# Performance work log

Hardware: AMD Instinct MI355X
Metric: run time of the kernel (lower is better)

Reference implementation:

```python
import jax, jax.numpy as jnp
import numpy as np

B, N, K = 4, 4096, 16
DP, DM = 128, 256  # d_points, d_model


def setup_inputs() -> dict:
    key = jax.random.key(0)
    ks = jax.random.split(key, 10)
    w = lambda k, s: (jax.random.normal(k, s) * 0.02).astype(jnp.float32)
    return dict(
        features=jax.random.normal(ks[0], (B, N, DP), dtype=jnp.float32),
        xyz=jax.random.normal(ks[1], (B, N, 3), dtype=jnp.float32),
        fc1_w=w(ks[2], (DP, DM)), fc1_b=jnp.zeros((DM,), jnp.float32),
        fc2_w=w(ks[3], (DM, DP)), fc2_b=jnp.zeros((DP,), jnp.float32),
        fd1_w=w(ks[4], (3, DM)), fd1_b=jnp.zeros((DM,), jnp.float32),
        fd2_w=w(ks[5], (DM, DM)), fd2_b=jnp.zeros((DM,), jnp.float32),
        wq=w(ks[6], (DM, DM)), wk=w(ks[7], (DM, DM)), wv=w(ks[8], (DM, DM)),
    )


def reference(features, xyz, fc1_w, fc1_b, fc2_w, fc2_b,
              fd1_w, fd1_b, fd2_w, fd2_b, wq, wk, wv):
    # KNN of xyz against itself (includes self, distance-sorted ascending)
    sq = jnp.sum(xyz * xyz, axis=-1)                                 # [B,N]
    d2 = sq[:, :, None] + sq[:, None, :] - 2.0 * jnp.einsum('bnc,bmc->bnm', xyz, xyz)
    _, knn_idx = jax.lax.top_k(-d2, K)                               # [B,N,K]
    gather = jax.vmap(lambda pts, idx: pts[idx])                     # [B,N,C],[B,N,K]->[B,N,K,C]
    knn_xyz = gather(xyz, knn_idx)                                   # [B,N,K,3]

    x = features @ fc1_w + fc1_b                                     # [B,N,DM]
    q = x @ wq                                                       # [B,N,DM]
    kf = gather(x @ wk, knn_idx)                                     # [B,N,K,DM]
    vf = gather(x @ wv, knn_idx)                                     # [B,N,K,DM]

    delta = xyz[:, :, None, :] - knn_xyz                             # [B,N,K,3]
    pos = jax.nn.relu(delta @ fd1_w + fd1_b) @ fd2_w + fd2_b         # [B,N,K,DM]

    logits = jnp.einsum('bnd,bnkd->bnk', q, kf + pos) / np.sqrt(DM).astype(np.float32)
    attn = jax.nn.softmax(logits, axis=-1)                           # [B,N,K]
    res = jnp.einsum('bnk,bnkd->bnd', attn, vf + pos)                # [B,N,DM]

    out = res @ fc2_w + fc2_b + features                             # [B,N,DP]
    return jnp.transpose(out, (0, 2, 1))                             # [B,DP,N]
```

## Files before the change

kernel.cpp:

```cpp
#include <hip/hip_runtime.h>
#include <hip/hip_bf16.h>
#include <math.h>

#define B_   4
#define N_   4096
#define K_   16
#define DP_  128
#define DM_  256
#define NPTS (B_ * N_)
#define SEG_ 16
#define CAND_ (N_ / SEG_)
#define QPAD 136

typedef unsigned int u32;
typedef unsigned char u8;
typedef _Float16 f16;
typedef __attribute__((ext_vector_type(2))) __fp16 h2;
typedef __attribute__((ext_vector_type(8))) _Float16 f16x8;
typedef __attribute__((ext_vector_type(4))) float floatx4;

static __device__ __forceinline__ h2 pkrtz(float a, float b) {
    return __builtin_amdgcn_cvt_pkrtz(a, b);
}
static __device__ __forceinline__ u32 asu32(h2 h) { return __builtin_bit_cast(u32, h); }
static __device__ __forceinline__ h2 ash2(u32 u) { return __builtin_bit_cast(h2, u); }

#define CEXA(x, y) { u32 _lo = min(x, y); y = max(x, y); x = _lo; }
#define CEXD(x, y) { u32 _hi = max(x, y); y = min(x, y); x = _hi; }

static __device__ __forceinline__ void sort16_desc(u32 c[16]) {
    CEXD(c[0],c[1]);  CEXA(c[2],c[3]);  CEXD(c[4],c[5]);  CEXA(c[6],c[7]);
    CEXD(c[8],c[9]);  CEXA(c[10],c[11]); CEXD(c[12],c[13]); CEXA(c[14],c[15]);

    CEXD(c[0],c[2]);  CEXD(c[1],c[3]);  CEXA(c[4],c[6]);  CEXA(c[5],c[7]);
    CEXD(c[8],c[10]); CEXD(c[9],c[11]); CEXA(c[12],c[14]); CEXA(c[13],c[15]);
    CEXD(c[0],c[1]);  CEXD(c[2],c[3]);  CEXA(c[4],c[5]);  CEXA(c[6],c[7]);
    CEXD(c[8],c[9]);  CEXD(c[10],c[11]); CEXA(c[12],c[13]); CEXA(c[14],c[15]);

    CEXD(c[0],c[4]);  CEXD(c[1],c[5]);  CEXD(c[2],c[6]);  CEXD(c[3],c[7]);
    CEXA(c[8],c[12]); CEXA(c[9],c[13]); CEXA(c[10],c[14]); CEXA(c[11],c[15]);
    CEXD(c[0],c[2]);  CEXD(c[1],c[3]);  CEXD(c[4],c[6]);  CEXD(c[5],c[7]);
    CEXA(c[8],c[10]); CEXA(c[9],c[11]); CEXA(c[12],c[14]); CEXA(c[13],c[15]);
    CEXD(c[0],c[1]);  CEXD(c[2],c[3]);  CEXD(c[4],c[5]);  CEXD(c[6],c[7]);
    CEXA(c[8],c[9]);  CEXA(c[10],c[11]); CEXA(c[12],c[13]); CEXA(c[14],c[15]);

    CEXD(c[0],c[8]);  CEXD(c[1],c[9]);  CEXD(c[2],c[10]); CEXD(c[3],c[11]);
    CEXD(c[4],c[12]); CEXD(c[5],c[13]); CEXD(c[6],c[14]); CEXD(c[7],c[15]);
    CEXD(c[0],c[4]);  CEXD(c[1],c[5]);  CEXD(c[2],c[6]);  CEXD(c[3],c[7]);
    CEXD(c[8],c[12]); CEXD(c[9],c[13]); CEXD(c[10],c[14]); CEXD(c[11],c[15]);
    CEXD(c[0],c[2]);  CEXD(c[1],c[3]);  CEXD(c[4],c[6]);  CEXD(c[5],c[7]);
    CEXD(c[8],c[10]); CEXD(c[9],c[11]); CEXD(c[12],c[14]); CEXD(c[13],c[15]);
    CEXD(c[0],c[1]);  CEXD(c[2],c[3]);  CEXD(c[4],c[5]);  CEXD(c[6],c[7]);
    CEXD(c[8],c[9]);  CEXD(c[10],c[11]); CEXD(c[12],c[13]); CEXD(c[14],c[15]);
}

static __device__ __forceinline__ void remerge16_asc(u32 L[16]) {
    CEXA(L[0],L[8]);  CEXA(L[1],L[9]);  CEXA(L[2],L[10]); CEXA(L[3],L[11]);
    CEXA(L[4],L[12]); CEXA(L[5],L[13]); CEXA(L[6],L[14]); CEXA(L[7],L[15]);
    CEXA(L[0],L[4]);  CEXA(L[1],L[5]);  CEXA(L[2],L[6]);  CEXA(L[3],L[7]);
    CEXA(L[8],L[12]); CEXA(L[9],L[13]); CEXA(L[10],L[14]); CEXA(L[11],L[15]);
    CEXA(L[0],L[2]);  CEXA(L[1],L[3]);  CEXA(L[4],L[6]);  CEXA(L[5],L[7]);
    CEXA(L[8],L[10]); CEXA(L[9],L[11]); CEXA(L[12],L[14]); CEXA(L[13],L[15]);
    CEXA(L[0],L[1]);  CEXA(L[2],L[3]);  CEXA(L[4],L[5]);  CEXA(L[6],L[7]);
    CEXA(L[8],L[9]);  CEXA(L[10],L[11]); CEXA(L[12],L[13]); CEXA(L[14],L[15]);
}

static __device__ void knn_part_body(float4* sc, const float* __restrict__ xyz,
                                     u32* __restrict__ part, int id)
{
    const int xblk = id & 15;
    const int s = (id >> 4) & 15;
    const int b = id >> 8;
    const int n = xblk * 256 + threadIdx.x;
    const float* xb = xyz + (size_t)b * N_ * 3;
    const float nx0 = -xb[n * 3 + 0], nx1 = -xb[n * 3 + 1], nx2 = -xb[n * 3 + 2];
    const u32 kmask = 0xFFFFF000u;

    {
        const int m = s * CAND_ + threadIdx.x;
        const float a0 = xb[m * 3 + 0];
        const float a1 = xb[m * 3 + 1];
        const float a2 = xb[m * 3 + 2];
        sc[threadIdx.x] = make_float4(a0, a1, a2, 0.5f * (a0 * a0 + a1 * a1 + a2 * a2));
    }
    __syncthreads();

    u32 L[16];
#pragma unroll
    for (int i = 0; i < 16; ++i) L[i] = 0xFFFFFFFFu;

    const u32 ibase = (u32)(s * CAND_);
    for (int m0 = 0; m0 < CAND_; m0 += 16) {
        u32 c[16];
#pragma unroll
        for (int t = 0; t < 16; ++t) {
            const float4 cc = sc[m0 + t];
            const float e = fmaf(nx0, cc.x, fmaf(nx1, cc.y, fmaf(nx2, cc.z, cc.w)));
            const int ib = __float_as_int(e);
            const u32 tk = (u32)ib ^ (u32)((ib >> 31) | 0x80000000);
            c[t] = (tk & kmask) | (ibase + (u32)(m0 + t));
        }
        sort16_desc(c);
#pragma unroll
        for (int i = 0; i < 16; ++i) L[i] = min(L[i], c[i]);
        remerge16_asc(L);
    }

    const int p = b * N_ + n;
#pragma unroll
    for (int j = 0; j < 16; ++j)
        part[(size_t)(s * 16 + j) * NPTS + p] = L[j];
}

static __device__ void prep_body(float (*t)[33],
    const float* __restrict__ wq, const float* __restrict__ wk, const float* __restrict__ wv,
    const float* __restrict__ fd2, const float* __restrict__ fc1, const float* __restrict__ fc2,
    const float* __restrict__ feat,
    f16* __restrict__ catW, f16* __restrict__ fc2T, f16* __restrict__ bt2,
    f16* __restrict__ fd2c, f16* __restrict__ wqc, f16* __restrict__ fc1c,
    f16* __restrict__ featb, int bx, int by, int job)
{
    const int tid = threadIdx.x;

    if (job < 4) {
        const float* in; int R, C;
        switch (job) {
            case 0: in = wq;  R = DM_; C = DM_; break;
            case 1: in = wk;  R = DM_; C = DM_; break;
            case 2: in = wv;  R = DM_; C = DM_; break;
            default: in = fc2; R = DM_; C = DP_; break;
        }
        const int c0 = bx * 32, r0 = by * 32;
        if (c0 >= C || r0 >= R) return;
        const int lx = tid & 31, ly = tid >> 5;
#pragma unroll
        for (int i = 0; i < 32; i += 8)
            t[ly + i][lx] = in[(size_t)(r0 + ly + i) * C + c0 + lx];
        __syncthreads();
#pragma unroll
        for (int i = 0; i < 32; i += 8) {
            const int c = c0 + ly + i;
            const f16 v = (f16)t[lx][ly + i];
            int n;
            switch (job) {
                case 0: n = c; break;
                case 1: n = 256 + ((c >> 2) << 3) + (c & 3); break;
                case 2: n = 256 + ((c >> 2) << 3) + 4 + (c & 3); break;
                default: n = -1; break;
            }
            if (job < 3) {
                catW[(size_t)n * DM_ + r0 + lx] = v;
            } else {
                fc2T[(size_t)c * DM_ + r0 + lx] = v;
                bt2[(size_t)c * 512 + 256 + r0 + lx] = v;
            }
        }
    } else {
        const int bid = by * 8 + bx;
        const int tId = bid * 256 + tid;
        const float* in; f16* outp; int n4;
        if (job == 4)      { in = fd2;  outp = fd2c;  n4 = (DM_ * DM_) / 4; }
        else if (job == 5) { in = wq;   outp = wqc;   n4 = (DM_ * DM_) / 4; }
        else if (job == 6) { in = fc1;  outp = fc1c;  n4 = (DP_ * DM_) / 4; }
        else               { in = feat; outp = featb; n4 = (NPTS * DP_) / 4; }
        for (int i = tId; i < n4; i += 16384) {
            const float4 v = ((const float4*)in)[i];
            const u32 lo = asu32(pkrtz(v.x, v.y));
            const u32 hi = asu32(pkrtz(v.z, v.w));
            ((uint2*)outp)[i] = make_uint2(lo, hi);
        }
    }
}

__global__ __launch_bounds__(256) void fused_prep_knn_kernel(
    const float* __restrict__ wq, const float* __restrict__ wk, const float* __restrict__ wv,
    const float* __restrict__ fd2, const float* __restrict__ fc1, const float* __restrict__ fc2,
    const float* __restrict__ feat,
    f16* __restrict__ catW, f16* __restrict__ fc2T, f16* __restrict__ bt2,
    f16* __restrict__ fd2c, f16* __restrict__ wqc, f16* __restrict__ fc1c,
    f16* __restrict__ featb,
    const float* __restrict__ xyz, u32* __restrict__ part)
{
    __shared__ __align__(16) char smem[4352];
    const int id = blockIdx.x;
    if (id < 512) {
        prep_body((float(*)[33])smem, wq, wk, wv, fd2, fc1, fc2, feat,
                  catW, fc2T, bt2, fd2c, wqc, fc1c, featb,
                  id & 7, (id >> 3) & 7, id >> 6);
    } else {
        knn_part_body((float4*)smem, xyz, part, id - 512);
    }
}

static __device__ void gemm_tile(f16* As, f16* Bs,
    const f16* __restrict__ A, const f16* __restrict__ Bt,
    f16* __restrict__ Cb,
    int M, int N, int K, int ldc, int bx, int by)
{
    const int tid = threadIdx.x;
    const int m0 = by * 128, n0 = bx * 128;
    const int w = tid >> 6, l = tid & 63;
    const int wm = (w >> 1) * 64, wn = (w & 1) * 64;
    const int fm = l & 15, kq = l >> 4;

    floatx4 acc[4][4];
#pragma unroll
    for (int i = 0; i < 4; ++i)
#pragma unroll
        for (int j = 0; j < 4; ++j)
            acc[i][j] = (floatx4){0.0f, 0.0f, 0.0f, 0.0f};

    for (int k0 = 0; k0 < K; k0 += 32) {
        __syncthreads();
#pragma unroll
        for (int c = 0; c < 2; ++c) {
            const int li = tid + c * 256;
            const int row = li >> 2, part = li & 3;
            *(uint4*)&As[row * 32 + part * 8] =
                *(const uint4*)&A[(size_t)(m0 + row) * K + k0 + part * 8];
            *(uint4*)&Bs[row * 32 + part * 8] =
                *(const uint4*)&Bt[(size_t)(n0 + row) * K + k0 + part * 8];
        }
        __syncthreads();
        f16x8 af[4], bf[4];
#pragma unroll
        for (int i = 0; i < 4; ++i)
            af[i] = *(const f16x8*)&As[(wm + i * 16 + fm) * 32 + kq * 8];
#pragma unroll
        for (int j = 0; j < 4; ++j)
            bf[j] = *(const f16x8*)&Bs[(wn + j * 16 + fm) * 32 + kq * 8];
#pragma unroll
        for (int i = 0; i < 4; ++i)
#pragma unroll
            for (int j = 0; j < 4; ++j)
                acc[i][j] = __builtin_amdgcn_mfma_f32_16x16x32_f16(af[i], bf[j], acc[i][j], 0, 0, 0);
    }

#pragma unroll
    for (int i = 0; i < 4; ++i) {
#pragma unroll
        for (int j = 0; j < 4; ++j) {
            const int col = n0 + wn + j * 16 + fm;
            const int rowb = m0 + wm + i * 16 + kq * 4;
#pragma unroll
            for (int r = 0; r < 4; ++r)
                Cb[(size_t)(rowb + r) * ldc + col] = (f16)acc[i][j][r];
        }
    }
}

__global__ __launch_bounds__(256) void gemm_qkv_kernel(
    const f16* __restrict__ A,
    const f16* __restrict__ Bt,
    const float* __restrict__ bias,
    f16* __restrict__ Cb)
{
    __shared__ __align__(16) f16 As[128 * QPAD];
    __shared__ __align__(16) f16 Bs[128 * QPAD];
    const int tid = threadIdx.x;
    const int m0 = blockIdx.y * 128, n0 = blockIdx.x * 128;
    const int w = tid >> 6, l = tid & 63;
    const int wm = (w >> 1) * 64, wn = (w & 1) * 64;
    const int fm = l & 15, kq = l >> 4;

#pragma unroll
    for (int c = 0; c < 8; ++c) {
        const int li = tid + c * 256;
        const int row = li >> 4, part = li & 15;
        *(uint4*)&As[row * QPAD + part * 8] =
            *(const uint4*)&A[(size_t)(m0 + row) * 128 + part * 8];
        *(uint4*)&Bs[row * QPAD + part * 8] =
            *(const uint4*)&Bt[(size_t)(n0 + row) * 128 + part * 8];
    }
    __syncthreads();

    floatx4 acc[4][4];
#pragma unroll
    for (int i = 0; i < 4; ++i)
#pragma unroll
        for (int j = 0; j < 4; ++j)
            acc[i][j] = (floatx4){0.0f, 0.0f, 0.0f, 0.0f};

#pragma unroll
    for (int kk = 0; kk < 4; ++kk) {
        f16x8 af[4], bf[4];
#pragma unroll
        for (int i = 0; i < 4; ++i)
            af[i] = *(const f16x8*)&As[(wm + i * 16 + fm) * QPAD + kk * 32 + kq * 8];
#pragma unroll
        for (int j = 0; j < 4; ++j)
            bf[j] = *(const f16x8*)&Bs[(wn + j * 16 + fm) * QPAD + kk * 32 + kq * 8];
#pragma unroll
        for (int i = 0; i < 4; ++i)
#pragma unroll
            for (int j = 0; j < 4; ++j)
                acc[i][j] = __builtin_amdgcn_mfma_f32_16x16x32_f16(af[i], bf[j], acc[i][j], 0, 0, 0);
    }

#pragma unroll
    for (int i = 0; i < 4; ++i) {
#pragma unroll
        for (int j = 0; j < 4; ++j) {
            const int col = n0 + wn + j * 16 + fm;
            const int rowb = m0 + wm + i * 16 + kq * 4;
#pragma unroll
            for (int r = 0; r < 4; ++r)
                Cb[(size_t)(rowb + r) * 1024 + col] = (f16)(acc[i][j][r] + bias[col]);
        }
    }
}

__global__ __launch_bounds__(256) void gemm_out_kernel(
    const f16* __restrict__ A,
    const f16* __restrict__ Bt,
    const float* __restrict__ bias2,
    const float* __restrict__ feat,
    float* __restrict__ CT)
{
    __shared__ __align__(16) f16 As[64 * 32];
    __shared__ __align__(16) f16 Bs[128 * 32];
    const int tid = threadIdx.x;
    const int m0 = blockIdx.x * 64;
    const int w = tid >> 6, l = tid & 63;
    const int wn = w * 32;
    const int fm = l & 15, kq = l >> 4;

    floatx4 acc[4][2];
#pragma unroll
    for (int i = 0; i < 4; ++i)
#pragma unroll
        for (int j = 0; j < 2; ++j)
            acc[i][j] = (floatx4){0.0f, 0.0f, 0.0f, 0.0f};

    for (int k0 = 0; k0 < 512; k0 += 32) {
        __syncthreads();
        {
            const int row = tid >> 2, part = tid & 3;
            *(uint4*)&As[row * 32 + part * 8] =
                *(const uint4*)&A[(size_t)(m0 + row) * 512 + k0 + part * 8];
        }
#pragma unroll
        for (int c = 0; c < 2; ++c) {
            const int li = tid + c * 256;
            const int row = li >> 2, part = li & 3;
            *(uint4*)&Bs[row * 32 + part * 8] =
                *(const uint4*)&Bt[(size_t)row * 512 + k0 + part * 8];
        }
        __syncthreads();
        f16x8 af[4], bf[2];
#pragma unroll
        for (int i = 0; i < 4; ++i)
            af[i] = *(const f16x8*)&As[(i * 16 + fm) * 32 + kq * 8];
#pragma unroll
        for (int j = 0; j < 2; ++j)
            bf[j] = *(const f16x8*)&Bs[(wn + j * 16 + fm) * 32 + kq * 8];
#pragma unroll
        for (int i = 0; i < 4; ++i)
#pragma unroll
            for (int j = 0; j < 2; ++j)
                acc[i][j] = __builtin_amdgcn_mfma_f32_16x16x32_f16(af[i], bf[j], acc[i][j], 0, 0, 0);
    }

#pragma unroll
    for (int i = 0; i < 4; ++i) {
#pragma unroll
        for (int j = 0; j < 2; ++j) {
            const int col = wn + j * 16 + fm;
            const int rowb = m0 + i * 16 + kq * 4;
            float4 vv;
#pragma unroll
            for (int r = 0; r < 4; ++r)
                ((float*)&vv)[r] = acc[i][j][r] + bias2[col]
                                 + feat[(size_t)(rowb + r) * DP_ + col];
            const int bb = rowb >> 12;
            *(float4*)&CT[(size_t)(bb * DP_ + col) * N_ + (rowb & (N_ - 1))] = vv;
        }
    }
}

static __device__ void kv8_body(const f16* __restrict__ qkv, u8* __restrict__ kv8, int id)
{
    const int t = id * 256 + threadIdx.x;
    const int p = t >> 6, g = t & 63;
    const uint4 kv = *(const uint4*)(qkv + (size_t)p * 1024 + 256 + g * 8);
    const h2 k01 = ash2(kv.x), k23 = ash2(kv.y), v01 = ash2(kv.z), v23 = ash2(kv.w);
    int lo = 0, hi = 0;
    lo = __builtin_amdgcn_cvt_pk_fp8_f32((float)k01.x, (float)k01.y, lo, false);
    lo = __builtin_amdgcn_cvt_pk_fp8_f32((float)k23.x, (float)k23.y, lo, true);
    hi = __builtin_amdgcn_cvt_pk_fp8_f32((float)v01.x, (float)v01.y, hi, false);
    hi = __builtin_amdgcn_cvt_pk_fp8_f32((float)v23.x, (float)v23.y, hi, true);
    *(uint2*)(kv8 + (size_t)p * 512 + g * 8) = make_uint2((u32)lo, (u32)hi);
}

static __device__ void mergeAB_body(const u32* __restrict__ part, int* __restrict__ knn_idx,
                                    int id)
{
    const int p = id * 256 + threadIdx.x;
    const int b = p >> 12;

    u32 L[16];
#pragma unroll
    for (int i = 0; i < 16; ++i) L[i] = 0xFFFFFFFFu;

    for (int s = 0; s < SEG_; ++s) {
        u32 seg[16];
#pragma unroll
        for (int j = 0; j < 16; ++j)
            seg[j] = part[(size_t)(s * 16 + j) * NPTS + p];
#pragma unroll
        for (int i = 0; i < 16; ++i) L[i] = min(L[i], seg[15 - i]);
        remerge16_asc(L);
    }

    int* o = knn_idx + (size_t)p * K_;
#pragma unroll
    for (int i = 0; i < 16; ++i) o[i] = b * N_ + (int)(L[i] & 0xFFFu);
}

__global__ __launch_bounds__(256) void fused_kv8merge_kernel(
    const f16* __restrict__ qkv, u8* __restrict__ kv8,
    const u32* __restrict__ part, int* __restrict__ knn_idx)
{
    const int id = blockIdx.x;
    if (id < NPTS * 64 / 256) kv8_body(qkv, kv8, id);
    else                      mergeAB_body(part, knn_idx, id - NPTS * 64 / 256);
}

__global__ __launch_bounds__(256) void fused_small1_kernel(
    const f16* __restrict__ fd2c, const f16* __restrict__ wqc,
    f16* __restrict__ catWqp,
    const f16* __restrict__ fc2T, f16* __restrict__ bt2)
{
    __shared__ __align__(16) f16 As[128 * 32];
    __shared__ __align__(16) f16 Bs[128 * 32];
    const int id = blockIdx.x;
    if (id < 4)
        gemm_tile(As, Bs, fd2c, wqc, catWqp, DM_, DM_, DM_, DM_, id & 1, id >> 1);
    else
        gemm_tile(As, Bs, fc2T, fd2c, bt2, DP_, DM_, DM_, 512, id - 4, 0);
}

__global__ __launch_bounds__(256) void fused_small2_kernel(
    const f16* __restrict__ catW, const f16* __restrict__ fc1c, f16* __restrict__ WallT,
    const float* __restrict__ fc1_b, const float* __restrict__ fd2_b,
    const float* __restrict__ fc2_w, const float* __restrict__ fc2_b,
    float* __restrict__ b_all, float* __restrict__ bias2)
{
    __shared__ __align__(16) f16 As[128 * 32];
    __shared__ __align__(16) f16 Bs[128 * 32];
    const int id = blockIdx.x;
    const int tid = threadIdx.x;
    if (id < 8) {
        gemm_tile(As, Bs, catW, fc1c, WallT, 1024, DP_, DM_, DP_, 0, id);
    } else if (id < 12) {
        const int n = (id - 8) * 256 + tid;
        float s = 0.0f;
        for (int j = 0; j < DM_; ++j)
            s += fc1_b[j] * (float)catW[(size_t)n * DM_ + j];
        b_all[n] = s;
    } else if (tid < DP_) {
        float s = fc2_b[tid];
        for (int t = 0; t < DM_; ++t)
            s += fd2_b[t] * fc2_w[(size_t)t * DP_ + tid];
        bias2[tid] = s;
    }
}

__global__ __launch_bounds__(256, 1) void attn_kernel(
    const float* __restrict__ xyz, const f16* __restrict__ qkv,
    const u8* __restrict__ kv8, const int* __restrict__ knn_idx,
    const float* __restrict__ fd1_w, const float* __restrict__ fd1_b,
    const float* __restrict__ fd2_b,
    f16* __restrict__ ab)
{
    const int wave = threadIdx.x >> 6, l = threadIdx.x & 63;
    const int bi = blockIdx.x;
    const int p = ((bi & 3) << 12) + ((bi >> 2) << 2) + wave;
    const int c0 = l * 4;

    int gi = 0; float dx = 0.0f, dy = 0.0f, dz = 0.0f;
    if (l < 16) {
        gi = knn_idx[p * K_ + l];
        dx = xyz[(size_t)p * 3 + 0] - xyz[(size_t)gi * 3 + 0];
        dy = xyz[(size_t)p * 3 + 1] - xyz[(size_t)gi * 3 + 1];
        dz = xyz[(size_t)p * 3 + 2] - xyz[(size_t)gi * 3 + 2];
    }

    uint2 kvr8[16];
#pragma unroll
    for (int k = 0; k < 16; ++k) {
        const int gik = __shfl(gi, k);
        kvr8[k] = *(const uint2*)(kv8 + (size_t)gik * 512 + l * 8);
    }
    asm volatile("" ::: "memory");

    const uint2 qu  = *(const uint2*)(qkv + (size_t)p * 1024 + c0);
    const uint2 qpu = *(const uint2*)(qkv + (size_t)p * 1024 + 768 + c0);
    const h2 qh01 = ash2(qu.x), qh23 = ash2(qu.y);
    const h2 qph01 = ash2(qpu.x), qph23 = ash2(qpu.y);
    const float q0 = (float)qh01.x, q1 = (float)qh01.y, q2 = (float)qh23.x, q3 = (float)qh23.y;
    const float qp0 = (float)qph01.x, qp1 = (float)qph01.y, qp2 = (float)qph23.x, qp3 = (float)qph23.y;

    const float4 w0 = *(const float4*)&fd1_w[c0];
    const float4 w1 = *(const float4*)&fd1_w[DM_ + c0];
    const float4 w2 = *(const float4*)&fd1_w[2 * DM_ + c0];
    const float4 b1 = *(const float4*)&fd1_b[c0];
    const float4 f2b = *(const float4*)&fd2_b[c0];

    float qb;
    {
        float tq = q0 * f2b.x + q1 * f2b.y + q2 * f2b.z + q3 * f2b.w;
#pragma unroll
        for (int off = 1; off < 64; off <<= 1) tq += __shfl_xor(tq, off);
        qb = tq;
    }

    float lg[16];
    u32 h01r[16], h23r[16];
#pragma unroll
    for (int k = 0; k < 16; ++k) {
        const float d0 = __shfl(dx, k), d1 = __shfl(dy, k), d2 = __shfl(dz, k);
        const float h0 = fmaxf(d0 * w0.x + d1 * w1.x + d2 * w2.x + b1.x, 0.0f);
        const float h1 = fmaxf(d0 * w0.y + d1 * w1.y + d2 * w2.y + b1.y, 0.0f);
        const float h2v = fmaxf(d0 * w0.z + d1 * w1.z + d2 * w2.z + b1.z, 0.0f);
        const float h3 = fmaxf(d0 * w0.w + d1 * w1.w + d2 * w2.w + b1.w, 0.0f);
        h01r[k] = asu32(pkrtz(h0, h1));
        h23r[k] = asu32(pkrtz(h2v, h3));
        const auto k01 = __builtin_amdgcn_cvt_pk_f32_fp8((int)kvr8[k].x, false);
        const auto k23 = __builtin_amdgcn_cvt_pk_f32_fp8((int)kvr8[k].x, true);
        float t = q0 * k01[0] + q1 * k01[1] + q2 * k23[0] + q3 * k23[1]
                + h0 * qp0 + h1 * qp1 + h2v * qp2 + h3 * qp3;
#pragma unroll
        for (int off = 1; off < 64; off <<= 1) t += __shfl_xor(t, off);
        lg[k] = t;
    }

    float att[16];
    {
        float mx = -3.0e38f;
#pragma unroll
        for (int k = 0; k < 16; ++k) {
            att[k] = (lg[k] + qb) * (1.0f / 16.0f);
            mx = fmaxf(mx, att[k]);
        }
        float s = 0.0f;
#pragma unroll
        for (int k = 0; k < 16; ++k) { att[k] = __expf(att[k] - mx); s += att[k]; }
        const float inv = 1.0f / s;
#pragma unroll
        for (int k = 0; k < 16; ++k) att[k] *= inv;
    }

    float rb[4] = {0, 0, 0, 0}, hb[4] = {0, 0, 0, 0};
#pragma unroll
    for (int k = 0; k < 16; ++k) {
        const auto v01 = __builtin_amdgcn_cvt_pk_f32_fp8((int)kvr8[k].y, false);
        const auto v23 = __builtin_amdgcn_cvt_pk_f32_fp8((int)kvr8[k].y, true);
        const h2 hh01 = ash2(h01r[k]), hh23 = ash2(h23r[k]);
        const float a = att[k];
        rb[0] = fmaf(a, v01[0], rb[0]);
        rb[1] = fmaf(a, v01[1], rb[1]);
        rb[2] = fmaf(a, v23[0], rb[2]);
        rb[3] = fmaf(a, v23[1], rb[3]);
        hb[0] = fmaf(a, (float)hh01.x, hb[0]);
        hb[1] = fmaf(a, (float)hh01.y, hb[1]);
        hb[2] = fmaf(a, (float)hh23.x, hb[2]);
        hb[3] = fmaf(a, (float)hh23.y, hb[3]);
    }

    const uint2 ho = make_uint2(asu32(pkrtz(hb[0], hb[1])), asu32(pkrtz(hb[2], hb[3])));
    const uint2 ro = make_uint2(asu32(pkrtz(rb[0], rb[1])), asu32(pkrtz(rb[2], rb[3])));
    *(uint2*)(ab + (size_t)p * 512 + c0) = ho;
    *(uint2*)(ab + (size_t)p * 512 + 256 + c0) = ro;
}

extern "C" void kernel_launch(void* const* d_in, const int* in_sizes, int n_in,
                              void* d_out, int out_size, void* d_ws, size_t ws_size,
                              hipStream_t stream)
{
    const float* features = (const float*)d_in[0];
    const float* xyz   = (const float*)d_in[1];
    const float* fc1_w = (const float*)d_in[2];
    const float* fc1_b = (const float*)d_in[3];
    const float* fc2_w = (const float*)d_in[4];
    const float* fc2_b = (const float*)d_in[5];
    const float* fd1_w = (const float*)d_in[6];
    const float* fd1_b = (const float*)d_in[7];
    const float* fd2_w = (const float*)d_in[8];
    const float* fd2_b = (const float*)d_in[9];
    const float* wq    = (const float*)d_in[10];
    const float* wk    = (const float*)d_in[11];
    const float* wv    = (const float*)d_in[12];
    float* out = (float*)d_out;

    char* base = (char*)d_ws;
    const size_t MB = 1024 * 1024;
    u32*  part = (u32*)(base + 0);
    f16*  ab   = (f16*)(base + 0);
    u8*   kv8  = (u8*)(base + 20 * MB);
    f16*  qkv  = (f16*)(base + 36 * MB);
    f16*  featb = (f16*)(base + 68 * MB);
    int*  idx  = (int*)(base + 72 * MB);
    char* wb = base + 73 * MB;
    f16* catW  = (f16*)(wb + 0);
    f16* WallT = (f16*)(wb + 512 * 1024);
    f16* bt2   = (f16*)(wb + 768 * 1024);
    f16* fd2c  = (f16*)(wb + 896 * 1024);
    f16* wqc   = (f16*)(wb + 1024 * 1024);
    f16* fc1c  = (f16*)(wb + 1152 * 1024);
    f16* fc2T  = (f16*)(wb + 1216 * 1024);
    float* b_all = (float*)(wb + 1280 * 1024);
    float* bias2 = (float*)(wb + 1284 * 1024);

    const dim3 blk(256);

    fused_prep_knn_kernel<<<dim3(512 + 1024), blk, 0, stream>>>(
        wq, wk, wv, fd2_w, fc1_w, fc2_w, features,
        catW, fc2T, bt2, fd2c, wqc, fc1c, featb, xyz, part);
    fused_small1_kernel<<<dim3(6), blk, 0, stream>>>(fd2c, wqc, catW + 768 * 256, fc2T, bt2);
    fused_small2_kernel<<<dim3(13), blk, 0, stream>>>(catW, fc1c, WallT,
                                                      fc1_b, fd2_b, fc2_w, fc2_b, b_all, bias2);
    gemm_qkv_kernel<<<dim3(1024 / 128, NPTS / 128), blk, 0, stream>>>(featb, WallT, b_all, qkv);
    fused_kv8merge_kernel<<<dim3(NPTS * 64 / 256 + NPTS / 256), blk, 0, stream>>>(
        qkv, kv8, part, idx);
    attn_kernel<<<dim3(NPTS / 4), blk, 0, stream>>>(xyz, qkv, kv8, idx,
                                                    fd1_w, fd1_b, fd2_b, ab);
    gemm_out_kernel<<<dim3(NPTS / 64), blk, 0, stream>>>(ab, bt2, bias2, features, out);

    (void)in_sizes; (void)n_in; (void)out_size; (void)ws_size;
}
```

Before: 223.2 us.

## Precompute per-point fd1 projections and evaluate position MLP layer in packed fp16

Uses linearity of the first position-MLP layer: (xi - xj)·W = xi·W - xj·W. Each point's projection xj·W is computed once in the kv conversion pass and stored next to its fp8 K/V, and the query-side term xi·W + b goes into a separate buffer. In the attention kernel the per-neighbor hidden layer then becomes a packed fp16 subtract and max, followed by fdot2 for the logit contribution. This removes the per-neighbor xyz gathers and fp32 FMAs, but doubles the gathered bytes per neighbor (16 instead of 8) and computes the hidden activations at fp16 precision.

```diff
diff --git a/kernel.cpp b/kernel.cpp
--- a/kernel.cpp
+++ b/kernel.cpp
@@ -1,5 +1,6 @@
 #include <hip/hip_runtime.h>
 #include <hip/hip_bf16.h>
+#include <hip/hip_fp16.h>
 #include <math.h>
 
 #define B_   4
@@ -378,7 +379,9 @@
     }
 }
 
-static __device__ void kv8_body(const f16* __restrict__ qkv, u8* __restrict__ kv8, int id)
+static __device__ void kvw_body(const f16* __restrict__ qkv, const float* __restrict__ xyz,
+                                const float* __restrict__ fd1_w, const float* __restrict__ fd1_b,
+                                u8* __restrict__ kvw, f16* __restrict__ ubuf, int id)
 {
     const int t = id * 256 + threadIdx.x;
     const int p = t >> 6, g = t & 63;
@@ -389,7 +392,30 @@
     lo = __builtin_amdgcn_cvt_pk_fp8_f32((float)k23.x, (float)k23.y, lo, true);
     hi = __builtin_amdgcn_cvt_pk_fp8_f32((float)v01.x, (float)v01.y, hi, false);
     hi = __builtin_amdgcn_cvt_pk_fp8_f32((float)v23.x, (float)v23.y, hi, true);
-    *(uint2*)(kv8 + (size_t)p * 512 + g * 8) = make_uint2((u32)lo, (u32)hi);
+
+    const float x0 = xyz[(size_t)p * 3 + 0];
+    const float x1 = xyz[(size_t)p * 3 + 1];
+    const float x2 = xyz[(size_t)p * 3 + 2];
+    const int c0 = g * 4;
+    const float4 w0v = *(const float4*)&fd1_w[c0];
+    const float4 w1v = *(const float4*)&fd1_w[DM_ + c0];
+    const float4 w2v = *(const float4*)&fd1_w[2 * DM_ + c0];
+    const float4 b1v = *(const float4*)&fd1_b[c0];
+    const float ww0 = x0 * w0v.x + x1 * w1v.x + x2 * w2v.x;
+    const float ww1 = x0 * w0v.y + x1 * w1v.y + x2 * w2v.y;
+    const float ww2 = x0 * w0v.z + x1 * w1v.z + x2 * w2v.z;
+    const float ww3 = x0 * w0v.w + x1 * w1v.w + x2 * w2v.w;
+
+    uint4 row;
+    row.x = (u32)lo;
+    row.y = (u32)hi;
+    row.z = asu32(pkrtz(ww0, ww1));
+    row.w = asu32(pkrtz(ww2, ww3));
+    *(uint4*)(kvw + (size_t)p * 1024 + g * 16) = row;
+
+    const uint2 uu = make_uint2(asu32(pkrtz(ww0 + b1v.x, ww1 + b1v.y)),
+                                asu32(pkrtz(ww2 + b1v.z, ww3 + b1v.w)));
+    *(uint2*)(ubuf + (size_t)p * 256 + c0) = uu;
 }
 
 static __device__ void mergeAB_body(const u32* __restrict__ part, int* __restrict__ knn_idx,
@@ -417,12 +443,14 @@
     for (int i = 0; i < 16; ++i) o[i] = b * N_ + (int)(L[i] & 0xFFFu);
 }
 
-__global__ __launch_bounds__(256) void fused_kv8merge_kernel(
-    const f16* __restrict__ qkv, u8* __restrict__ kv8,
+__global__ __launch_bounds__(256) void fused_kvwmerge_kernel(
+    const f16* __restrict__ qkv, const float* __restrict__ xyz,
+    const float* __restrict__ fd1_w, const float* __restrict__ fd1_b,
+    u8* __restrict__ kvw, f16* __restrict__ ubuf,
     const u32* __restrict__ part, int* __restrict__ knn_idx)
 {
     const int id = blockIdx.x;
-    if (id < NPTS * 64 / 256) kv8_body(qkv, kv8, id);
+    if (id < NPTS * 64 / 256) kvw_body(qkv, xyz, fd1_w, fd1_b, kvw, ubuf, id);
     else                      mergeAB_body(part, knn_idx, id - NPTS * 64 / 256);
 }
 
@@ -467,9 +495,8 @@
 }
 
 __global__ __launch_bounds__(256, 1) void attn_kernel(
-    const float* __restrict__ xyz, const f16* __restrict__ qkv,
-    const u8* __restrict__ kv8, const int* __restrict__ knn_idx,
-    const float* __restrict__ fd1_w, const float* __restrict__ fd1_b,
+    const f16* __restrict__ qkv, const u8* __restrict__ kvw,
+    const f16* __restrict__ ubuf, const int* __restrict__ knn_idx,
     const float* __restrict__ fd2_b,
     f16* __restrict__ ab)
 {
@@ -478,33 +505,26 @@
     const int p = ((bi & 3) << 12) + ((bi >> 2) << 2) + wave;
     const int c0 = l * 4;
 
-    int gi = 0; float dx = 0.0f, dy = 0.0f, dz = 0.0f;
-    if (l < 16) {
-        gi = knn_idx[p * K_ + l];
-        dx = xyz[(size_t)p * 3 + 0] - xyz[(size_t)gi * 3 + 0];
-        dy = xyz[(size_t)p * 3 + 1] - xyz[(size_t)gi * 3 + 1];
-        dz = xyz[(size_t)p * 3 + 2] - xyz[(size_t)gi * 3 + 2];
-    }
-
-    uint2 kvr8[16];
+    int gi = 0;
+    if (l < 16) gi = knn_idx[p * K_ + l];
+
+    uint4 kvr[16];
 #pragma unroll
     for (int k = 0; k < 16; ++k) {
         const int gik = __shfl(gi, k);
-        kvr8[k] = *(const uint2*)(kv8 + (size_t)gik * 512 + l * 8);
+        kvr[k] = *(const uint4*)(kvw + (size_t)gik * 1024 + l * 16);
     }
     asm volatile("" ::: "memory");
 
     const uint2 qu  = *(const uint2*)(qkv + (size_t)p * 1024 + c0);
     const uint2 qpu = *(const uint2*)(qkv + (size_t)p * 1024 + 768 + c0);
+    const uint2 uu  = *(const uint2*)(ubuf + (size_t)p * 256 + c0);
     const h2 qh01 = ash2(qu.x), qh23 = ash2(qu.y);
-    const h2 qph01 = ash2(qpu.x), qph23 = ash2(qpu.y);
+    const h2 qp01 = ash2(qpu.x), qp23 = ash2(qpu.y);
+    const h2 u01 = ash2(uu.x), u23 = ash2(uu.y);
     const float q0 = (float)qh01.x, q1 = (float)qh01.y, q2 = (float)qh23.x, q3 = (float)qh23.y;
-    const float qp0 = (float)qph01.x, qp1 = (float)qph01.y, qp2 = (float)qph23.x, qp3 = (float)qph23.y;
-
-    const float4 w0 = *(const float4*)&fd1_w[c0];
-    const float4 w1 = *(const float4*)&fd1_w[DM_ + c0];
-    const float4 w2 = *(const float4*)&fd1_w[2 * DM_ + c0];
-    const float4 b1 = *(const float4*)&fd1_b[c0];
+    const h2 zero2 = (h2)(__fp16)0.0f;
+
     const float4 f2b = *(const float4*)&fd2_b[c0];
 
     float qb;
@@ -519,17 +539,17 @@
     u32 h01r[16], h23r[16];
 #pragma unroll
     for (int k = 0; k < 16; ++k) {
-        const float d0 = __shfl(dx, k), d1 = __shfl(dy, k), d2 = __shfl(dz, k);
-        const float h0 = fmaxf(d0 * w0.x + d1 * w1.x + d2 * w2.x + b1.x, 0.0f);
-        const float h1 = fmaxf(d0 * w0.y + d1 * w1.y + d2 * w2.y + b1.y, 0.0f);
-        const float h2v = fmaxf(d0 * w0.z + d1 * w1.z + d2 * w2.z + b1.z, 0.0f);
-        const float h3 = fmaxf(d0 * w0.w + d1 * w1.w + d2 * w2.w + b1.w, 0.0f);
-        h01r[k] = asu32(pkrtz(h0, h1));
-        h23r[k] = asu32(pkrtz(h2v, h3));
-        const auto k01 = __builtin_amdgcn_cvt_pk_f32_fp8((int)kvr8[k].x, false);
-        const auto k23 = __builtin_amdgcn_cvt_pk_f32_fp8((int)kvr8[k].x, true);
-        float t = q0 * k01[0] + q1 * k01[1] + q2 * k23[0] + q3 * k23[1]
-                + h0 * qp0 + h1 * qp1 + h2v * qp2 + h3 * qp3;
+        const uint4 r = kvr[k];
+        h2 d01 = u01 - ash2(r.z);
+        h2 d23 = u23 - ash2(r.w);
+        d01 = __builtin_elementwise_max(d01, zero2);
+        d23 = __builtin_elementwise_max(d23, zero2);
+        h01r[k] = asu32(d01); h23r[k] = asu32(d23);
+        const auto k01 = __builtin_amdgcn_cvt_pk_f32_fp8((int)r.x, false);
+        const auto k23 = __builtin_amdgcn_cvt_pk_f32_fp8((int)r.x, true);
+        float t = q0 * k01[0] + q1 * k01[1] + q2 * k23[0] + q3 * k23[1];
+        t = __builtin_amdgcn_fdot2(d01, qp01, t, false);
+        t = __builtin_amdgcn_fdot2(d23, qp23, t, false);
 #pragma unroll
         for (int off = 1; off < 64; off <<= 1) t += __shfl_xor(t, off);
         lg[k] = t;
@@ -554,8 +574,8 @@
     float rb[4] = {0, 0, 0, 0}, hb[4] = {0, 0, 0, 0};
 #pragma unroll
     for (int k = 0; k < 16; ++k) {
-        const auto v01 = __builtin_amdgcn_cvt_pk_f32_fp8((int)kvr8[k].y, false);
-        const auto v23 = __builtin_amdgcn_cvt_pk_f32_fp8((int)kvr8[k].y, true);
+        const auto v01 = __builtin_amdgcn_cvt_pk_f32_fp8((int)kvr[k].y, false);
+        const auto v23 = __builtin_amdgcn_cvt_pk_f32_fp8((int)kvr[k].y, true);
         const h2 hh01 = ash2(h01r[k]), hh23 = ash2(h23r[k]);
         const float a = att[k];
         rb[0] = fmaf(a, v01[0], rb[0]);
@@ -597,7 +617,7 @@
     const size_t MB = 1024 * 1024;
     u32*  part = (u32*)(base + 0);
     f16*  ab   = (f16*)(base + 0);
-    u8*   kv8  = (u8*)(base + 20 * MB);
+    u8*   kvw  = (u8*)(base + 20 * MB);
     f16*  qkv  = (f16*)(base + 36 * MB);
     f16*  featb = (f16*)(base + 68 * MB);
     int*  idx  = (int*)(base + 72 * MB);
@@ -611,6 +631,7 @@
     f16* fc2T  = (f16*)(wb + 1216 * 1024);
     float* b_all = (float*)(wb + 1280 * 1024);
     float* bias2 = (float*)(wb + 1284 * 1024);
+    f16*  ubuf = (f16*)(base + 76 * MB);
 
     const dim3 blk(256);
 
@@ -621,10 +642,9 @@
     fused_small2_kernel<<<dim3(13), blk, 0, stream>>>(catW, fc1c, WallT,
                                                       fc1_b, fd2_b, fc2_w, fc2_b, b_all, bias2);
     gemm_qkv_kernel<<<dim3(1024 / 128, NPTS / 128), blk, 0, stream>>>(featb, WallT, b_all, qkv);
-    fused_kv8merge_kernel<<<dim3(NPTS * 64 / 256 + NPTS / 256), blk, 0, stream>>>(
-        qkv, kv8, part, idx);
-    attn_kernel<<<dim3(NPTS / 4), blk, 0, stream>>>(xyz, qkv, kv8, idx,
-                                                    fd1_w, fd1_b, fd2_b, ab);
+    fused_kvwmerge_kernel<<<dim3(NPTS * 64 / 256 + NPTS / 256), blk, 0, stream>>>(
+        qkv, xyz, fd1_w, fd1_b, kvw, ubuf, part, idx);
+    attn_kernel<<<dim3(NPTS / 4), blk, 0, stream>>>(qkv, kvw, ubuf, idx, fd2_b, ab);
     gemm_out_kernel<<<dim3(NPTS / 64), blk, 0, stream>>>(ab, bt2, bias2, features, out);
 
     (void)in_sizes; (void)n_in; (void)out_size; (void)ws_size;
```

After: 214.1 us. 1.04x faster.
